# Optimization experiments

Measured on AMD Instinct MI355X. Metric: run time of the kernel, lower is better.

The kernel has to match this reference:

```python
import jax, jax.numpy as jnp
import numpy as np
from jax import lax

IMG = 800.0
PRE_NMS = 2000
POST_NMS = 1000
IOU_T = 0.7
BBOX_XFORM_CLIP = float(np.log(1000.0 / 16.0))


def build_anchors():
    # torchvision FPN anchor generator: one size per level, 3 aspect ratios
    strides = [4, 8, 16, 32, 64]
    sizes = [32, 64, 128, 256, 512]
    ratios = [0.5, 1.0, 2.0]
    out = []
    for s, sz in zip(strides, sizes):
        f = int(np.ceil(800 / s))  # feature map side
        base = []
        for r in ratios:
            w = sz * np.sqrt(1.0 / r)
            h = sz * np.sqrt(r)
            base.append([-w / 2, -h / 2, w / 2, h / 2])
        base = np.asarray(base)  # [3,4]
        sx = (np.arange(f) + 0.5) * s
        sy = (np.arange(f) + 0.5) * s
        yy, xx = np.meshgrid(sy, sx, indexing='ij')
        shifts = np.stack([xx, yy, xx, yy], -1).reshape(-1, 1, 4)
        out.append((shifts + base).reshape(-1, 4))
    return np.concatenate(out, 0).astype(np.float32)  # [159882,4]


def setup_inputs() -> dict:
    key = jax.random.key(0)
    k1, k2 = jax.random.split(key)
    B = 16
    anchors = jnp.asarray(build_anchors())
    A = anchors.shape[0]
    scores = jax.random.normal(k1, (B, A), dtype=jnp.float32)
    deltas = jax.random.normal(k2, (B, A, 4), dtype=jnp.float32) * 0.1
    return {"scores": scores, "deltas": deltas, "anchors": anchors}


def decode_boxes(deltas, anchors):
    wa = anchors[:, 2] - anchors[:, 0]
    ha = anchors[:, 3] - anchors[:, 1]
    cxa = anchors[:, 0] + 0.5 * wa
    cya = anchors[:, 1] + 0.5 * ha
    dx, dy = deltas[:, 0], deltas[:, 1]
    dw = jnp.minimum(deltas[:, 2], BBOX_XFORM_CLIP)
    dh = jnp.minimum(deltas[:, 3], BBOX_XFORM_CLIP)
    cx = dx * wa + cxa
    cy = dy * ha + cya
    w = jnp.exp(dw) * wa
    h = jnp.exp(dh) * ha
    boxes = jnp.stack([cx - 0.5 * w, cy - 0.5 * h, cx + 0.5 * w, cy + 0.5 * h], -1)
    return jnp.clip(boxes, 0.0, IMG)


def box_iou(a, b):
    # a: [N,4], b: [M,4]
    area_a = (a[:, 2] - a[:, 0]) * (a[:, 3] - a[:, 1])
    area_b = (b[:, 2] - b[:, 0]) * (b[:, 3] - b[:, 1])
    lt = jnp.maximum(a[:, None, :2], b[None, :, :2])
    rb = jnp.minimum(a[:, None, 2:], b[None, :, 2:])
    wh = jnp.clip(rb - lt, 0.0)
    inter = wh[..., 0] * wh[..., 1]
    return inter / (area_a[:, None] + area_b[None, :] - inter + 1e-9)


def greedy_nms_keep(boxes, iou_t):
    # boxes are sorted by descending score
    K = boxes.shape[0]
    iou = box_iou(boxes, boxes)  # [K,K]
    idx = jnp.arange(K)

    def body(i, keep):
        sup = (iou[i] > iou_t) & keep[i] & (idx > i)
        return keep & ~sup

    return lax.fori_loop(0, K, body, jnp.ones((K,), bool))


def _process_image(scores_i, deltas_i, anchors):
    # top-k pre-NMS on objectness logits (torchvision RPN order)
    top_logits, idx = lax.top_k(scores_i, PRE_NMS)
    boxes = decode_boxes(deltas_i[idx], anchors[idx])  # [PRE,4]
    keep = greedy_nms_keep(boxes, IOU_T)
    masked = jnp.where(keep, top_logits, -jnp.inf)
    kept_logits, idx2 = lax.top_k(masked, POST_NMS)
    kept_boxes = boxes[idx2]
    valid = jnp.isfinite(kept_logits)
    probs = jax.nn.sigmoid(jnp.where(valid, kept_logits, 0.0))
    out_boxes = jnp.where(valid[:, None], kept_boxes, 0.0)
    out_scores = jnp.where(valid, probs, 0.0)
    return jnp.concatenate([out_boxes, out_scores[:, None]], -1)  # [POST,5]


def reference(scores, deltas, anchors):
    return jax.vmap(_process_image, in_axes=(0, 0, None))(scores, deltas, anchors)
```

## Files before the change

kernel.cpp:

```cpp
#include <hip/hip_runtime.h>
#include <math.h>

#define PRE_NMS 2000
#define POST_NMS 1000
#define IOU_T 0.7f
#define IMGSZ 800.0f
#define CAP 6144
#define SORTN 2048
#define NBINS 1024
#define NWORDS 32
#define NSLICE 16
#define MROWS 2048
#define NTILES 528
#define TCAP 104

typedef unsigned long long u64;

__device__ __forceinline__ unsigned key_of(float f) {
    unsigned u = __float_as_uint(f);
    return (u & 0x80000000u) ? ~u : (u | 0x80000000u);
}
__device__ __forceinline__ float inv_key(unsigned k) {
    unsigned u = (k & 0x80000000u) ? (k ^ 0x80000000u) : ~k;
    return __uint_as_float(u);
}

__global__ __launch_bounds__(256) void hist_kernel(
    const float* __restrict__ scores, int A, unsigned* __restrict__ ghist,
    int* __restrict__ cand_cnt, unsigned* __restrict__ gwf) {
  int b = blockIdx.x, slice = blockIdx.y;
  __shared__ unsigned h[NBINS];
  int tid = threadIdx.x;
  for (int i = tid; i < NBINS; i += 256) h[i] = 0;
  if (slice == 0) {
    if (tid == 0) cand_cnt[b] = 0;
    if (tid < NWORDS) gwf[b * NWORDS + tid] = 0u;
  }
  __syncthreads();
  int per = (A + NSLICE - 1) / NSLICE;
  int lo = slice * per, hi = min(lo + per, A);
  const float* sc = scores + (size_t)b * A;
  for (int i = lo + tid; i < hi; i += 256)
    atomicAdd(&h[key_of(sc[i]) >> 22], 1u);
  __syncthreads();
  unsigned* gh = ghist + ((size_t)b * NSLICE + slice) * NBINS;
  for (int i = tid; i < NBINS; i += 256) gh[i] = h[i];
}

__global__ __launch_bounds__(256) void compact_kernel(
    const float* __restrict__ scores, int A, const unsigned* __restrict__ ghist,
    u64* __restrict__ cand, int* __restrict__ cand_cnt, int* __restrict__ T1) {
  int b = blockIdx.x, slice = blockIdx.y;
  int tid = threadIdx.x;
  int lane = tid & 63, wave = tid >> 6;
  __shared__ unsigned sa[2][NBINS];
  __shared__ int sT;
  for (int i = tid; i < NBINS; i += 256) {
    unsigned s = 0;
    const unsigned* gh = ghist + (size_t)b * NSLICE * NBINS + i;
    #pragma unroll
    for (int s16 = 0; s16 < NSLICE; ++s16) s += gh[s16 * NBINS];
    sa[0][i] = s;
  }
  __syncthreads();
  int src = 0;
  for (int d = 1; d < NBINS; d <<= 1) {
    for (int i = tid; i < NBINS; i += 256)
      sa[src ^ 1][i] = sa[src][i] + ((i + d < NBINS) ? sa[src][i + d] : 0u);
    __syncthreads();
    src ^= 1;
  }
  for (int i = tid; i < NBINS; i += 256) {
    unsigned v = sa[src][i];
    unsigned nx = (i < NBINS - 1) ? sa[src][i + 1] : 0u;
    if (v >= PRE_NMS && nx < PRE_NMS) sT = i;
  }
  __syncthreads();
  int T = sT;
  if (slice == 0 && tid == 0) T1[b] = T;
  int per = (A + NSLICE - 1) / NSLICE;
  int lo = slice * per, hi = min(lo + per, A);
  const float* sc = scores + (size_t)b * A;
  int cnt = 0;
  for (int i = lo + tid; i < hi; i += 256)
    cnt += ((int)(key_of(sc[i]) >> 22) >= T);
  int pfx = cnt;
  #pragma unroll
  for (int d = 1; d < 64; d <<= 1) {
    int t2 = __shfl_up(pfx, d, 64);
    if (lane >= d) pfx += t2;
  }
  __shared__ int s_wt[4];
  __shared__ int s_base;
  if (lane == 63) s_wt[wave] = pfx;
  __syncthreads();
  if (tid == 0) {
    int tot = s_wt[0] + s_wt[1] + s_wt[2] + s_wt[3];
    int acc = 0;
    #pragma unroll
    for (int w2 = 0; w2 < 4; ++w2) { int t3 = s_wt[w2]; s_wt[w2] = acc; acc += t3; }
    s_base = atomicAdd(&cand_cnt[b], tot);
  }
  __syncthreads();
  int my_off = s_base + s_wt[wave] + (pfx - cnt);
  u64* cb = cand + (size_t)b * CAP;
  for (int i = lo + tid; i < hi; i += 256) {
    unsigned k = key_of(sc[i]);
    if ((int)(k >> 22) >= T) {
      if (my_off < CAP) cb[my_off] = ((u64)k << 32) | (unsigned)(~i);
      my_off++;
    }
  }
}

__global__ __launch_bounds__(1024) void refine_select_kernel(
    const u64* __restrict__ cand, const int* __restrict__ cand_cnt,
    const int* __restrict__ T1,
    u64* __restrict__ gsel, int* __restrict__ sel_cnt) {
  int b = blockIdx.x, tid = threadIdx.x;
  int lane = tid & 63;
  __shared__ unsigned h2[NBINS];
  __shared__ unsigned tmp[NBINS];
  __shared__ int s_above, s_sel, s_T2;
  int n = min(cand_cnt[b], CAP);
  const u64* cb = cand + (size_t)b * CAP;
  h2[tid] = 0;
  if (tid == 0) { s_above = 0; s_sel = 0; }
  __syncthreads();
  int T1v = T1[b];
  int loc = 0;
  for (int i = tid; i < n; i += 1024) {
    unsigned k = (unsigned)(cb[i] >> 32);
    if ((int)(k >> 22) > T1v) loc++;
    else atomicAdd(&h2[(k >> 12) & 1023], 1u);
  }
  for (int d = 32; d; d >>= 1) loc += __shfl_down(loc, d, 64);
  if (lane == 0 && loc) atomicAdd(&s_above, loc);
  __syncthreads();
  unsigned v = h2[tid];
  for (int d = 1; d < NBINS; d <<= 1) {
    tmp[tid] = v;
    __syncthreads();
    if (tid + d < NBINS) v += tmp[tid + d];
    __syncthreads();
  }
  tmp[tid] = v;
  __syncthreads();
  int above = s_above;
  unsigned nextv = (tid < NBINS - 1) ? tmp[tid + 1] : 0u;
  if (above + (int)v >= PRE_NMS && above + (int)nextv < PRE_NMS) s_T2 = tid;
  __syncthreads();
  unsigned thresh20 = ((unsigned)T1v << 10) | (unsigned)s_T2;
  u64* gs = gsel + (size_t)b * SORTN;
  for (int i = tid; i < n; i += 1024) {
    u64 cv = cb[i];
    if ((unsigned)(cv >> 44) >= thresh20) {
      int pos = atomicAdd(&s_sel, 1);
      if (pos < SORTN) gs[pos] = cv;
    }
  }
  __syncthreads();
  if (tid == 0) sel_cnt[b] = min(s_sel, SORTN);
}

__global__ __launch_bounds__(256) void rank_decode_kernel(
    const u64* __restrict__ gsel, const int* __restrict__ sel_cnt,
    const float* __restrict__ deltas, const float* __restrict__ anchors, int A,
    float* __restrict__ boxes, float* __restrict__ topk_logit) {
  int b = blockIdx.x, ci = blockIdx.y;
  int tid = threadIdx.x;
  __shared__ u64 keys[SORTN];
  __shared__ int s_part[256];
  const u64* gs = gsel + (size_t)b * SORTN;
  int n = sel_cnt[b];
  for (int i = tid; i < SORTN; i += 256)
    keys[i] = (i < n) ? gs[i] : 0ULL;
  __syncthreads();
  int half = tid >> 7;
  int li = tid & 127;
  int i = ci * 128 + li;
  u64 my = keys[i];
  int rank = 0;
  const ulonglong2* k2 = (const ulonglong2*)(keys + half * (SORTN / 2));
  #pragma unroll 4
  for (int j = 0; j < SORTN / 4; ++j) {
    ulonglong2 kk = k2[j];
    rank += (kk.x > my) + (kk.y > my);
  }
  s_part[tid] = rank;
  __syncthreads();
  if (half == 0) {
    rank = s_part[tid] + s_part[tid + 128];
    if (i < n && rank < PRE_NMS) {
      int a = (int)(~(unsigned)my);
      topk_logit[b * PRE_NMS + rank] = inv_key((unsigned)(my >> 32));
      const float CLIP = 4.135166556742356f;
      float4 dl = ((const float4*)deltas)[(size_t)b * A + a];
      float4 an = ((const float4*)anchors)[a];
      float wa = __fsub_rn(an.z, an.x);
      float ha = __fsub_rn(an.w, an.y);
      float cxa = __fadd_rn(an.x, __fmul_rn(0.5f, wa));
      float cya = __fadd_rn(an.y, __fmul_rn(0.5f, ha));
      float dw = fminf(dl.z, CLIP), dh = fminf(dl.w, CLIP);
      float cx = __fadd_rn(__fmul_rn(dl.x, wa), cxa);
      float cy = __fadd_rn(__fmul_rn(dl.y, ha), cya);
      float w2 = __fmul_rn((float)exp((double)dw), wa);
      float h2f = __fmul_rn((float)exp((double)dh), ha);
      float x1 = __fsub_rn(cx, __fmul_rn(0.5f, w2));
      float y1 = __fsub_rn(cy, __fmul_rn(0.5f, h2f));
      float x2 = __fadd_rn(cx, __fmul_rn(0.5f, w2));
      float y2 = __fadd_rn(cy, __fmul_rn(0.5f, h2f));
      x1 = fminf(fmaxf(x1, 0.f), IMGSZ);
      y1 = fminf(fmaxf(y1, 0.f), IMGSZ);
      x2 = fminf(fmaxf(x2, 0.f), IMGSZ);
      y2 = fminf(fmaxf(y2, 0.f), IMGSZ);
      ((float4*)boxes)[(size_t)b * PRE_NMS + rank] = make_float4(x1, y1, x2, y2);
    }
  }
}

__global__ __launch_bounds__(64) void iou_tile(
    const float* __restrict__ boxes, u64* __restrict__ maskT,
    unsigned* __restrict__ gwf) {
  int k = blockIdx.x;
  int b = blockIdx.y;
  int wj = (int)((sqrtf(8.0f * k + 1.0f) - 1.0f) * 0.5f);
  while ((wj + 1) * (wj + 2) / 2 <= k) ++wj;
  while (wj * (wj + 1) / 2 > k) --wj;
  int ti = k - wj * (wj + 1) / 2;
  int lane = threadIdx.x;
  int i = ti * 64 + lane;
  const float4* bb = (const float4*)boxes + (size_t)b * PRE_NMS;
  __shared__ float4 sbox[64];
  int jg = wj * 64 + lane;
  sbox[lane] = bb[min(jg, PRE_NMS - 1)];
  float4 A4 = bb[min(i, PRE_NMS - 1)];
  __syncthreads();
  float area_a = __fmul_rn(__fsub_rn(A4.z, A4.x), __fsub_rn(A4.w, A4.y));
  u64 m = 0;
  #pragma unroll 8
  for (int jj = 0; jj < 64; ++jj) {
    float4 Bb = sbox[jj];
    float area_b = __fmul_rn(__fsub_rn(Bb.z, Bb.x), __fsub_rn(Bb.w, Bb.y));
    float ltx = fmaxf(A4.x, Bb.x), lty = fmaxf(A4.y, Bb.y);
    float rbx = fminf(A4.z, Bb.z), rby = fminf(A4.w, Bb.w);
    float iw = fmaxf(__fsub_rn(rbx, ltx), 0.f);
    float ih = fmaxf(__fsub_rn(rby, lty), 0.f);
    float inter = __fmul_rn(iw, ih);
    float denom = __fadd_rn(__fsub_rn(__fadd_rn(area_a, area_b), inter), 1e-9f);
    int j = wj * 64 + jj;
    if (j > i && inter > __fmul_rn(IOU_T, denom)) m |= 1ULL << jj;
  }
  u64 anyb = __ballot(m != 0ULL);
  if (anyb) {
    maskT[((size_t)b * NWORDS + wj) * MROWS + i] = m;
    if (lane == 0) atomicOr(&gwf[b * NWORDS + ti], 1u << wj);
  }
}

__global__ __launch_bounds__(256, 1) void nms_scan(
    const u64* __restrict__ maskT, const unsigned* __restrict__ gwf,
    const float* __restrict__ boxes,
    const float* __restrict__ logits, float* __restrict__ out) {
  int b = blockIdx.x;
  int tid = threadIdx.x;
  int lane = tid & 63, wave = tid >> 6;
  __shared__ u64 tiles[TCAP][64];
  __shared__ unsigned swf[NWORDS];
  __shared__ int wbase[NWORDS];
  __shared__ unsigned short slot2cw[TCAP];
  __shared__ int s_nact;
  __shared__ u64 s_keep[NWORDS];
  __shared__ int pre[NWORDS];
  __shared__ int s_tot;
  const u64* mb = maskT + (size_t)b * NWORDS * MROWS;
  if (tid < NWORDS) swf[tid] = gwf[b * NWORDS + tid];
  __syncthreads();
  if (tid == 0) {
    int s = 0;
    for (int c = 0; c < NWORDS; ++c) {
      wbase[c] = s;
      unsigned wf = swf[c];
      while (wf) {
        int w2 = __ffs(wf) - 1; wf &= wf - 1;
        if (s < TCAP) slot2cw[s] = (unsigned short)((w2 << 8) | c);
        s++;
      }
    }
    s_nact = s;
  }
  __syncthreads();
  int nstage = min(s_nact, TCAP);
  for (int g = tid; g < nstage * 64; g += 256) {
    int slot = g >> 6, r = g & 63;
    unsigned cw = slot2cw[slot];
    int c = cw & 0xFF, w2 = cw >> 8;
    tiles[slot][r] = mb[(size_t)w2 * MROWS + c * 64 + r];
  }
  __syncthreads();
  if (wave == 0) {
    u64 keep = (lane < NWORDS) ? ((lane == NWORDS - 1) ? 0xFFFFULL : ~0ULL) : 0ULL;
    unsigned wfreg = (lane < NWORDS) ? swf[lane] : 0u;
    int baser = (lane < NWORDS) ? wbase[lane] : 0;
    unsigned wmask = (unsigned)__ballot(wfreg != 0u);
    while (wmask) {
      int c = __ffs(wmask) - 1; wmask &= wmask - 1;
      unsigned wf = __shfl(wfreg, c, 64);
      int base = __shfl(baser, c, 64);
      u64 cur = __shfl(keep, c, 64);
      if ((wf >> c) & 1u) {
        int slot = base;
        u64 d = (slot < TCAP) ? tiles[slot][lane]
                              : mb[(size_t)c * MROWS + c * 64 + lane];
        unsigned dlo = (unsigned)d, dhi = (unsigned)(d >> 32);
        unsigned clo = __builtin_amdgcn_readfirstlane((unsigned)cur);
        unsigned chi = __builtin_amdgcn_readfirstlane((unsigned)(cur >> 32));
        #pragma unroll
        for (int bb = 0; bb < 32; ++bb) {
          unsigned rlo = __builtin_amdgcn_readlane(dlo, bb);
          unsigned rhi = __builtin_amdgcn_readlane(dhi, bb);
          unsigned msk = 0u - ((clo >> bb) & 1u);
          clo &= ~(rlo & msk);
          chi &= ~(rhi & msk);
        }
        #pragma unroll
        for (int bb = 0; bb < 32; ++bb) {
          unsigned rlo = __builtin_amdgcn_readlane(dlo, bb + 32);
          unsigned rhi = __builtin_amdgcn_readlane(dhi, bb + 32);
          unsigned msk = 0u - ((chi >> bb) & 1u);
          clo &= ~(rlo & msk);
          chi &= ~(rhi & msk);
        }
        cur = ((u64)chi << 32) | clo;
        keep = (lane == c) ? cur : keep;
      }
      unsigned rem = wf & ~(1u << c);
      while (rem) {
        int w2 = __ffs(rem) - 1; rem &= rem - 1;
        int slot = base + __popc(wf & ((1u << w2) - 1u));
        u64 row = (slot < TCAP) ? tiles[slot][lane]
                                : mb[(size_t)w2 * MROWS + c * 64 + lane];
        u64 bit = (cur >> lane) & 1ULL;
        u64 v = row & (0ULL - bit);
        u64 mnz = __ballot(v != 0ULL);
        u64 sv = 0;
        while (mnz) {
          int l = (int)__ffsll((long long)mnz) - 1; mnz &= mnz - 1;
          unsigned slo = __builtin_amdgcn_readlane((unsigned)v, l);
          unsigned shi = __builtin_amdgcn_readlane((unsigned)(v >> 32), l);
          sv |= ((u64)shi << 32) | slo;
        }
        keep = (lane == w2) ? (keep & ~sv) : keep;
      }
    }
    if (lane < NWORDS) s_keep[lane] = keep;
  }
  __syncthreads();
  if (tid == 0) {
    int acc = 0;
    for (int ww = 0; ww < NWORDS; ++ww) {
      pre[ww] = acc;
      acc += __popcll(s_keep[ww]);
    }
    s_tot = acc;
  }
  __syncthreads();
  const float* lg_b = logits + b * PRE_NMS;
  const float4* bx_b = (const float4*)boxes + (size_t)b * PRE_NMS;
  for (int i = tid; i < PRE_NMS; i += 256) {
    u64 wv = s_keep[i >> 6];
    if ((wv >> (i & 63)) & 1) {
      int rank = pre[i >> 6] + __popcll(wv & ((1ULL << (i & 63)) - 1ULL));
      if (rank < POST_NMS) {
        float4 bx = bx_b[i];
        float lg = lg_b[i];
        float e = (float)exp(-(double)lg);
        float pp = 1.0f / (1.0f + e);
        float* o = out + ((size_t)b * POST_NMS + rank) * 5;
        o[0] = bx.x; o[1] = bx.y; o[2] = bx.z; o[3] = bx.w; o[4] = pp;
      }
    }
  }
  int tot = s_tot;
  for (int j = tid; j < POST_NMS; j += 256) {
    if (j >= tot) {
      float* o = out + ((size_t)b * POST_NMS + j) * 5;
      o[0] = 0.f; o[1] = 0.f; o[2] = 0.f; o[3] = 0.f; o[4] = 0.f;
    }
  }
}

extern "C" void kernel_launch(void* const* d_in, const int* in_sizes, int n_in,
                              void* d_out, int out_size, void* d_ws, size_t ws_size,
                              hipStream_t stream) {
  const float* scores  = (const float*)d_in[0];
  const float* deltas  = (const float*)d_in[1];
  const float* anchors = (const float*)d_in[2];
  int A = in_sizes[2] / 4;
  int B = in_sizes[0] / A;

  char* ws = (char*)d_ws;
  size_t off = 0;
  auto alloc = [&](size_t bytes) {
    void* p = ws + off;
    off += (bytes + 255) & ~(size_t)255;
    return p;
  };
  unsigned* ghist    = (unsigned*)alloc((size_t)B * NSLICE * NBINS * 4);
  int*      cand_cnt = (int*)alloc((size_t)B * 4);
  int*      T1       = (int*)alloc((size_t)B * 4);
  u64*      cand     = (u64*)alloc((size_t)B * CAP * 8);
  u64*      gsel     = (u64*)alloc((size_t)B * SORTN * 8);
  int*      sel_cnt  = (int*)alloc((size_t)B * 4);
  float*    topk_lg  = (float*)alloc((size_t)B * PRE_NMS * 4);
  float*    boxes    = (float*)alloc((size_t)B * PRE_NMS * 16);
  u64*      maskT    = (u64*)alloc((size_t)B * NWORDS * MROWS * 8);
  unsigned* gwf      = (unsigned*)alloc((size_t)B * NWORDS * 4);

  hist_kernel<<<dim3(B, NSLICE), 256, 0, stream>>>(scores, A, ghist, cand_cnt, gwf);
  compact_kernel<<<dim3(B, NSLICE), 256, 0, stream>>>(scores, A, ghist, cand, cand_cnt, T1);
  refine_select_kernel<<<B, 1024, 0, stream>>>(cand, cand_cnt, T1, gsel, sel_cnt);
  rank_decode_kernel<<<dim3(B, SORTN / 128), 256, 0, stream>>>(
      gsel, sel_cnt, deltas, anchors, A, boxes, topk_lg);
  iou_tile<<<dim3(NTILES, B), 64, 0, stream>>>(boxes, maskT, gwf);
  nms_scan<<<B, 256, 0, stream>>>(maskT, gwf, boxes, topk_lg, (float*)d_out);
}
```

Measured before the change: 196.2 us.

## Fuse refine histogram into compact, wave-level threshold scan, pack IoU tiles per block

Replaces multi-barrier shared-memory suffix scans with a single-wave register/shuffle suffix scan for threshold finding. Builds the second-level histogram and above-count inside compact_kernel using global atomics, so refine_select no longer rescans candidates. Vectorizes score reads as float2 and packs four IoU tiles into one 256-thread block without a barrier. Risks include global atomic contention, reliance on intra-wave LDS visibility, and the assumption that A is even.

```diff
diff --git a/kernel.cpp b/kernel.cpp
--- a/kernel.cpp
+++ b/kernel.cpp
@@ -25,23 +25,56 @@
     return __uint_as_float(u);
 }
 
+__device__ __forceinline__ void wave_suffix_thresh(
+    const unsigned* __restrict__ h, int above, int lane, int* out_T) {
+  const uint4* h4 = (const uint4*)h;
+  uint4 q0 = h4[lane * 4 + 0];
+  uint4 q1 = h4[lane * 4 + 1];
+  uint4 q2 = h4[lane * 4 + 2];
+  uint4 q3 = h4[lane * 4 + 3];
+  unsigned v[16] = {q0.x, q0.y, q0.z, q0.w, q1.x, q1.y, q1.z, q1.w,
+                    q2.x, q2.y, q2.z, q2.w, q3.x, q3.y, q3.z, q3.w};
+  #pragma unroll
+  for (int j = 14; j >= 0; --j) v[j] += v[j + 1];
+  unsigned tot = v[0];
+  unsigned x = tot;
+  #pragma unroll
+  for (int d = 1; d < 64; d <<= 1) {
+    unsigned y = __shfl_down(x, d, 64);
+    if (lane + d < 64) x += y;
+  }
+  unsigned excl = x - tot;
+  #pragma unroll
+  for (int j = 0; j < 16; ++j) {
+    int cur = above + (int)(v[j] + excl);
+    int nxt = above + (int)(((j < 15) ? v[j + 1] : 0u) + excl);
+    if (cur >= PRE_NMS && nxt < PRE_NMS) *out_T = lane * 16 + j;
+  }
+}
+
 __global__ __launch_bounds__(256) void hist_kernel(
     const float* __restrict__ scores, int A, unsigned* __restrict__ ghist,
-    int* __restrict__ cand_cnt, unsigned* __restrict__ gwf) {
+    int* __restrict__ cand_cnt, unsigned* __restrict__ gwf,
+    unsigned* __restrict__ gh2, int* __restrict__ gabove) {
   int b = blockIdx.x, slice = blockIdx.y;
   __shared__ unsigned h[NBINS];
   int tid = threadIdx.x;
   for (int i = tid; i < NBINS; i += 256) h[i] = 0;
   if (slice == 0) {
-    if (tid == 0) cand_cnt[b] = 0;
+    if (tid == 0) { cand_cnt[b] = 0; gabove[b] = 0; }
     if (tid < NWORDS) gwf[b * NWORDS + tid] = 0u;
-  }
-  __syncthreads();
-  int per = (A + NSLICE - 1) / NSLICE;
-  int lo = slice * per, hi = min(lo + per, A);
-  const float* sc = scores + (size_t)b * A;
-  for (int i = lo + tid; i < hi; i += 256)
-    atomicAdd(&h[key_of(sc[i]) >> 22], 1u);
+    for (int i = tid; i < NBINS; i += 256) gh2[b * NBINS + i] = 0u;
+  }
+  __syncthreads();
+  int nc = A >> 1;
+  int per = (nc + NSLICE - 1) / NSLICE;
+  int lo = slice * per, hi = min(lo + per, nc);
+  const float2* sc2 = (const float2*)(scores + (size_t)b * A);
+  for (int c = lo + tid; c < hi; c += 256) {
+    float2 v = sc2[c];
+    atomicAdd(&h[key_of(v.x) >> 22], 1u);
+    atomicAdd(&h[key_of(v.y) >> 22], 1u);
+  }
   __syncthreads();
   unsigned* gh = ghist + ((size_t)b * NSLICE + slice) * NBINS;
   for (int i = tid; i < NBINS; i += 256) gh[i] = h[i];
@@ -49,41 +82,35 @@
 
 __global__ __launch_bounds__(256) void compact_kernel(
     const float* __restrict__ scores, int A, const unsigned* __restrict__ ghist,
-    u64* __restrict__ cand, int* __restrict__ cand_cnt, int* __restrict__ T1) {
+    u64* __restrict__ cand, int* __restrict__ cand_cnt, int* __restrict__ T1,
+    unsigned* __restrict__ gh2, int* __restrict__ gabove) {
   int b = blockIdx.x, slice = blockIdx.y;
   int tid = threadIdx.x;
   int lane = tid & 63, wave = tid >> 6;
-  __shared__ unsigned sa[2][NBINS];
+  __shared__ __align__(16) unsigned h[NBINS];
   __shared__ int sT;
   for (int i = tid; i < NBINS; i += 256) {
     unsigned s = 0;
     const unsigned* gh = ghist + (size_t)b * NSLICE * NBINS + i;
     #pragma unroll
     for (int s16 = 0; s16 < NSLICE; ++s16) s += gh[s16 * NBINS];
-    sa[0][i] = s;
-  }
-  __syncthreads();
-  int src = 0;
-  for (int d = 1; d < NBINS; d <<= 1) {
-    for (int i = tid; i < NBINS; i += 256)
-      sa[src ^ 1][i] = sa[src][i] + ((i + d < NBINS) ? sa[src][i + d] : 0u);
-    __syncthreads();
-    src ^= 1;
-  }
-  for (int i = tid; i < NBINS; i += 256) {
-    unsigned v = sa[src][i];
-    unsigned nx = (i < NBINS - 1) ? sa[src][i + 1] : 0u;
-    if (v >= PRE_NMS && nx < PRE_NMS) sT = i;
-  }
+    h[i] = s;
+  }
+  __syncthreads();
+  if (wave == 0) wave_suffix_thresh(h, 0, lane, &sT);
   __syncthreads();
   int T = sT;
   if (slice == 0 && tid == 0) T1[b] = T;
-  int per = (A + NSLICE - 1) / NSLICE;
-  int lo = slice * per, hi = min(lo + per, A);
-  const float* sc = scores + (size_t)b * A;
+  int nc = A >> 1;
+  int per = (nc + NSLICE - 1) / NSLICE;
+  int lo = slice * per, hi = min(lo + per, nc);
+  const float2* sc2 = (const float2*)(scores + (size_t)b * A);
   int cnt = 0;
-  for (int i = lo + tid; i < hi; i += 256)
-    cnt += ((int)(key_of(sc[i]) >> 22) >= T);
+  for (int c = lo + tid; c < hi; c += 256) {
+    float2 v = sc2[c];
+    cnt += ((int)(key_of(v.x) >> 22) >= T);
+    cnt += ((int)(key_of(v.y) >> 22) >= T);
+  }
   int pfx = cnt;
   #pragma unroll
   for (int d = 1; d < 64; d <<= 1) {
@@ -104,55 +131,47 @@
   __syncthreads();
   int my_off = s_base + s_wt[wave] + (pfx - cnt);
   u64* cb = cand + (size_t)b * CAP;
-  for (int i = lo + tid; i < hi; i += 256) {
-    unsigned k = key_of(sc[i]);
-    if ((int)(k >> 22) >= T) {
-      if (my_off < CAP) cb[my_off] = ((u64)k << 32) | (unsigned)(~i);
-      my_off++;
-    }
-  }
-}
-
-__global__ __launch_bounds__(1024) void refine_select_kernel(
+  int na = 0;
+  for (int c = lo + tid; c < hi; c += 256) {
+    float2 v = sc2[c];
+    unsigned kk[2] = {key_of(v.x), key_of(v.y)};
+    #pragma unroll
+    for (int j = 0; j < 2; ++j) {
+      unsigned k = kk[j];
+      if ((int)(k >> 22) >= T) {
+        if (my_off < CAP) {
+          cb[my_off] = ((u64)k << 32) | (unsigned)(~(2 * c + j));
+          if ((int)(k >> 22) > T) na++;
+          else atomicAdd(&gh2[b * NBINS + ((k >> 12) & 1023)], 1u);
+        }
+        my_off++;
+      }
+    }
+  }
+  #pragma unroll
+  for (int d = 32; d; d >>= 1) na += __shfl_down(na, d, 64);
+  if (lane == 0 && na) atomicAdd(&gabove[b], na);
+}
+
+__global__ __launch_bounds__(256) void refine_select_kernel(
     const u64* __restrict__ cand, const int* __restrict__ cand_cnt,
-    const int* __restrict__ T1,
+    const int* __restrict__ T1, const unsigned* __restrict__ gh2,
+    const int* __restrict__ gabove,
     u64* __restrict__ gsel, int* __restrict__ sel_cnt) {
   int b = blockIdx.x, tid = threadIdx.x;
-  int lane = tid & 63;
-  __shared__ unsigned h2[NBINS];
-  __shared__ unsigned tmp[NBINS];
-  __shared__ int s_above, s_sel, s_T2;
+  int lane = tid & 63, wave = tid >> 6;
+  __shared__ __align__(16) unsigned h2[NBINS];
+  __shared__ int s_sel, s_T2;
+  for (int i = tid; i < NBINS; i += 256) h2[i] = gh2[b * NBINS + i];
+  if (tid == 0) s_sel = 0;
+  __syncthreads();
+  if (wave == 0) wave_suffix_thresh(h2, gabove[b], lane, &s_T2);
+  __syncthreads();
+  unsigned thresh20 = ((unsigned)T1[b] << 10) | (unsigned)s_T2;
   int n = min(cand_cnt[b], CAP);
   const u64* cb = cand + (size_t)b * CAP;
-  h2[tid] = 0;
-  if (tid == 0) { s_above = 0; s_sel = 0; }
-  __syncthreads();
-  int T1v = T1[b];
-  int loc = 0;
-  for (int i = tid; i < n; i += 1024) {
-    unsigned k = (unsigned)(cb[i] >> 32);
-    if ((int)(k >> 22) > T1v) loc++;
-    else atomicAdd(&h2[(k >> 12) & 1023], 1u);
-  }
-  for (int d = 32; d; d >>= 1) loc += __shfl_down(loc, d, 64);
-  if (lane == 0 && loc) atomicAdd(&s_above, loc);
-  __syncthreads();
-  unsigned v = h2[tid];
-  for (int d = 1; d < NBINS; d <<= 1) {
-    tmp[tid] = v;
-    __syncthreads();
-    if (tid + d < NBINS) v += tmp[tid + d];
-    __syncthreads();
-  }
-  tmp[tid] = v;
-  __syncthreads();
-  int above = s_above;
-  unsigned nextv = (tid < NBINS - 1) ? tmp[tid + 1] : 0u;
-  if (above + (int)v >= PRE_NMS && above + (int)nextv < PRE_NMS) s_T2 = tid;
-  __syncthreads();
-  unsigned thresh20 = ((unsigned)T1v << 10) | (unsigned)s_T2;
   u64* gs = gsel + (size_t)b * SORTN;
-  for (int i = tid; i < n; i += 1024) {
+  for (int i = tid; i < n; i += 256) {
     u64 cv = cb[i];
     if ((unsigned)(cv >> 44) >= thresh20) {
       int pos = atomicAdd(&s_sel, 1);
@@ -219,28 +238,28 @@
   }
 }
 
-__global__ __launch_bounds__(64) void iou_tile(
+__global__ __launch_bounds__(256) void iou_tile(
     const float* __restrict__ boxes, u64* __restrict__ maskT,
     unsigned* __restrict__ gwf) {
-  int k = blockIdx.x;
   int b = blockIdx.y;
+  int tid = threadIdx.x;
+  int lane = tid & 63, wave = tid >> 6;
+  int k = blockIdx.x * 4 + wave;
   int wj = (int)((sqrtf(8.0f * k + 1.0f) - 1.0f) * 0.5f);
   while ((wj + 1) * (wj + 2) / 2 <= k) ++wj;
   while (wj * (wj + 1) / 2 > k) --wj;
   int ti = k - wj * (wj + 1) / 2;
-  int lane = threadIdx.x;
   int i = ti * 64 + lane;
   const float4* bb = (const float4*)boxes + (size_t)b * PRE_NMS;
-  __shared__ float4 sbox[64];
+  __shared__ float4 sbox[4][64];
   int jg = wj * 64 + lane;
-  sbox[lane] = bb[min(jg, PRE_NMS - 1)];
+  sbox[wave][lane] = bb[min(jg, PRE_NMS - 1)];
   float4 A4 = bb[min(i, PRE_NMS - 1)];
-  __syncthreads();
   float area_a = __fmul_rn(__fsub_rn(A4.z, A4.x), __fsub_rn(A4.w, A4.y));
   u64 m = 0;
   #pragma unroll 8
   for (int jj = 0; jj < 64; ++jj) {
-    float4 Bb = sbox[jj];
+    float4 Bb = sbox[wave][jj];
     float area_b = __fmul_rn(__fsub_rn(Bb.z, Bb.x), __fsub_rn(Bb.w, Bb.y));
     float ltx = fmaxf(A4.x, Bb.x), lty = fmaxf(A4.y, Bb.y);
     float rbx = fminf(A4.z, Bb.z), rby = fminf(A4.w, Bb.w);
@@ -416,12 +435,17 @@
   float*    boxes    = (float*)alloc((size_t)B * PRE_NMS * 16);
   u64*      maskT    = (u64*)alloc((size_t)B * NWORDS * MROWS * 8);
   unsigned* gwf      = (unsigned*)alloc((size_t)B * NWORDS * 4);
-
-  hist_kernel<<<dim3(B, NSLICE), 256, 0, stream>>>(scores, A, ghist, cand_cnt, gwf);
-  compact_kernel<<<dim3(B, NSLICE), 256, 0, stream>>>(scores, A, ghist, cand, cand_cnt, T1);
-  refine_select_kernel<<<B, 1024, 0, stream>>>(cand, cand_cnt, T1, gsel, sel_cnt);
+  unsigned* gh2      = (unsigned*)alloc((size_t)B * NBINS * 4);
+  int*      gabove   = (int*)alloc((size_t)B * 4);
+
+  hist_kernel<<<dim3(B, NSLICE), 256, 0, stream>>>(
+      scores, A, ghist, cand_cnt, gwf, gh2, gabove);
+  compact_kernel<<<dim3(B, NSLICE), 256, 0, stream>>>(
+      scores, A, ghist, cand, cand_cnt, T1, gh2, gabove);
+  refine_select_kernel<<<B, 256, 0, stream>>>(
+      cand, cand_cnt, T1, gh2, gabove, gsel, sel_cnt);
   rank_decode_kernel<<<dim3(B, SORTN / 128), 256, 0, stream>>>(
       gsel, sel_cnt, deltas, anchors, A, boxes, topk_lg);
-  iou_tile<<<dim3(NTILES, B), 64, 0, stream>>>(boxes, maskT, gwf);
+  iou_tile<<<dim3(NTILES / 4, B), 256, 0, stream>>>(boxes, maskT, gwf);
   nms_scan<<<B, 256, 0, stream>>>(maskT, gwf, boxes, topk_lg, (float*)d_out);
 }
```

Measured after the change: 200.8 us. +2.3%, slower.
